# Performance work log

Hardware: AMD Instinct MI355X
Metric: run time of the kernel (lower is better)

Reference implementation:

```python
import jax, jax.numpy as jnp
import numpy as np

GRID_SIZE = 5
SPLINE_ORDER = 3
GRID_RANGE = (-1.0, 1.0)
BATCH, IN_FEATURES, OUT_FEATURES = 8192, 512, 512


def make_grid():
    h = (GRID_RANGE[1] - GRID_RANGE[0]) / GRID_SIZE
    n = GRID_SIZE + 2 * SPLINE_ORDER + 1  # 12 knots
    return jnp.linspace(GRID_RANGE[0] - SPLINE_ORDER * h,
                        GRID_RANGE[1] + SPLINE_ORDER * h,
                        n, dtype=jnp.float32)


def b_spline(x, grid, k=SPLINE_ORDER):
    # Cox-de Boor recursion. x: (B, in) -> basis: (B, in, grid_size + k)
    x = x[..., None]                     # (B, in, 1)
    g = grid[None, None, :]              # (1, 1, n_knots)
    basis = ((x >= g[..., :-1]) & (x < g[..., 1:])).astype(x.dtype)
    for p in range(1, k + 1):
        left_denom = g[..., p:-1] - g[..., :-(p + 1)]
        right_denom = g[..., p + 1:] - g[..., 1:-p]
        left_denom = jnp.where(left_denom > 0, left_denom, jnp.ones_like(left_denom))
        right_denom = jnp.where(right_denom > 0, right_denom, jnp.ones_like(right_denom))
        left = (x - g[..., :-(p + 1)]) / left_denom * basis[..., :-1]
        right = (g[..., p + 1:] - x) / right_denom * basis[..., 1:]
        basis = left + right
    return basis


def setup_inputs() -> dict:
    key = jax.random.key(0)
    k1, k2, k3 = jax.random.split(key, 3)
    # x uniform in grid_range so spline basis is active
    x = jax.random.uniform(k1, (BATCH, IN_FEATURES), jnp.float32, minval=-1.0, maxval=1.0)
    # kaiming_uniform-like init for base weight
    bound = 1.0 / np.sqrt(IN_FEATURES)
    base_weight = jax.random.uniform(k2, (OUT_FEATURES, IN_FEATURES), jnp.float32,
                                     minval=-bound, maxval=bound)
    spline_weight = jax.random.normal(k3, (OUT_FEATURES, IN_FEATURES,
                                           GRID_SIZE + SPLINE_ORDER), jnp.float32) * 0.1
    return {"x": x, "base_weight": base_weight, "spline_weight": spline_weight}


def reference(x, base_weight, spline_weight):
    grid = make_grid()
    scale_base, scale_spline = 1.0, 1.0
    base_out = x @ base_weight.T                         # (B, out)
    basis = b_spline(x, grid, SPLINE_ORDER)              # (B, in, G+k)
    spline_out = jnp.einsum('bil,oil->bo', basis, spline_weight)
    return scale_base * base_out + scale_spline * spline_out
```

## Files before the change

### kernel.cpp

```cpp
#include <hip/hip_runtime.h>
#include <stdint.h>

typedef _Float16 half8 __attribute__((ext_vector_type(8)));
typedef float floatx4 __attribute__((ext_vector_type(4)));
typedef uint32_t u32x4 __attribute__((ext_vector_type(4)));

#define BM 128
#define BN 128
#define BK 64
#define NT 512
#define KT_BASE 8
#define KT_TOTAL 72
#define IF 512
#define NF 512

__device__ __forceinline__ uint32_t swz(uint32_t b) {
  return b ^ (((b >> 7) & 7u) << 4);
}

__device__ __forceinline__ uint32_t pk(float a, float b) {
  return __builtin_bit_cast(uint32_t, __builtin_amdgcn_cvt_pkrtz(a, b));
}

__global__ __launch_bounds__(NT, 2)
void kan_fused(const float* __restrict__ xg, const float* __restrict__ bwg,
               const float* __restrict__ swg, float* __restrict__ outg)
{
  __shared__ _Float16 As[BM * BK];
  __shared__ _Float16 Bs[BN * BK];

  const int tid = threadIdx.x;
  const int lane = tid & 63;
  const int wv = tid >> 6;
  const int wm = wv >> 2;
  const int wn = wv & 3;

  const int bid = blockIdx.x;
  const int lb = (bid & 7) * 32 + (bid >> 3);
  const int bm0 = (lb & 63) * BM;
  const int bn0 = (lb >> 6) * BN;

  const int rT = tid >> 3;
  const int c8 = (tid & 7) * 8;
  const int ii = tid & 7;
  const uint32_t wA0 = swz((uint32_t)rT * 128u + (uint32_t)c8 * 2u);
  const uint32_t wA1 = swz((uint32_t)(rT + 64) * 128u + (uint32_t)c8 * 2u);

  char* AsB = (char*)As;
  char* BsB = (char*)Bs;

  uint32_t rdA[4], rdB[2];
  {
    const int rr = lane & 15;
    const uint32_t cc = (uint32_t)(lane >> 4) * 16u;
#pragma unroll
    for (int mi = 0; mi < 4; ++mi)
      rdA[mi] = swz((uint32_t)(wm * 64 + mi * 16 + rr) * 128u + cc);
#pragma unroll
    for (int ni = 0; ni < 2; ++ni)
      rdB[ni] = swz((uint32_t)(wn * 32 + ni * 16 + rr) * 128u + cc);
  }

  floatx4 acc[4][2];
#pragma unroll
  for (int mi = 0; mi < 4; ++mi)
#pragma unroll
    for (int ni = 0; ni < 2; ++ni)
      acc[mi][ni] = (floatx4){0.f, 0.f, 0.f, 0.f};

  float4 aL[4];
  float4 bL[4];
  float xv0, xv1;

  auto LOAD = [&](int kt) {
    if (kt < KT_BASE) {
      const int kb = kt * 64;
      const float* a0 = xg + (size_t)(bm0 + rT) * IF + kb + c8;
      const float* a1 = a0 + (size_t)64 * IF;
      aL[0] = ((const float4*)a0)[0]; aL[1] = ((const float4*)a0)[1];
      aL[2] = ((const float4*)a1)[0]; aL[3] = ((const float4*)a1)[1];
      const float* b0 = bwg + (size_t)(bn0 + rT) * IF + kb + c8;
      const float* b1 = b0 + (size_t)64 * IF;
      bL[0] = ((const float4*)b0)[0]; bL[1] = ((const float4*)b0)[1];
      bL[2] = ((const float4*)b1)[0]; bL[3] = ((const float4*)b1)[1];
    } else {
      const int ks = (kt - KT_BASE) * 64;
      const int i0 = ks >> 3;
      xv0 = xg[(size_t)(bm0 + rT) * IF + i0 + ii];
      xv1 = xg[(size_t)(bm0 + rT + 64) * IF + i0 + ii];
      const float* b0 = swg + (size_t)(bn0 + rT) * 4096 + ks + c8;
      const float* b1 = b0 + (size_t)64 * 4096;
      bL[0] = ((const float4*)b0)[0]; bL[1] = ((const float4*)b0)[1];
      bL[2] = ((const float4*)b1)[0]; bL[3] = ((const float4*)b1)[1];
    }
  };

  auto BASIS = [&](float xv) -> u32x4 {
    float u = (xv + 2.2f) * 2.5f;
    int j = (int)u;
    j = j < 3 ? 3 : (j > 7 ? 7 : j);
    float t = u - (float)j;
    float omt = 1.0f - t;
    float t2 = t * t, t3 = t2 * t;
    const float s6 = 0.16666666666666666f;
    float w0 = omt * omt * omt * s6;
    float w1 = (3.0f * t3 - 6.0f * t2 + 4.0f) * s6;
    float w2 = (-3.0f * t3 + 3.0f * t2 + 3.0f * t + 1.0f) * s6;
    float w3 = t3 * s6;
    uint32_t c0 = pk(w0, w1);
    uint32_t c1 = pk(w2, w3);
    const int j3 = j - 3;
    const bool odd = (j3 & 1) != 0;
    uint32_t lo  = odd ? (c0 << 16) : c0;
    uint32_t mid = odd ? ((c0 >> 16) | (c1 << 16)) : c1;
    uint32_t hi  = odd ? (c1 >> 16) : 0u;
    const int wofs = j3 >> 1;
    u32x4 r;
    r.x = (wofs == 0) ? lo : 0u;
    r.y = (wofs == 0) ? mid : ((wofs == 1) ? lo : 0u);
    r.z = (wofs == 0) ? hi : ((wofs == 1) ? mid : lo);
    r.w = (wofs == 1) ? hi : ((wofs == 2) ? mid : 0u);
    return r;
  };

  auto WRITE = [&](int kt) {
    if (kt < KT_BASE) {
      u32x4 v0; v0.x = pk(aL[0].x, aL[0].y); v0.y = pk(aL[0].z, aL[0].w);
                v0.z = pk(aL[1].x, aL[1].y); v0.w = pk(aL[1].z, aL[1].w);
      u32x4 v1; v1.x = pk(aL[2].x, aL[2].y); v1.y = pk(aL[2].z, aL[2].w);
                v1.z = pk(aL[3].x, aL[3].y); v1.w = pk(aL[3].z, aL[3].w);
      *(u32x4*)(AsB + wA0) = v0;
      *(u32x4*)(AsB + wA1) = v1;
    } else {
      *(u32x4*)(AsB + wA0) = BASIS(xv0);
      *(u32x4*)(AsB + wA1) = BASIS(xv1);
    }
    u32x4 u0; u0.x = pk(bL[0].x, bL[0].y); u0.y = pk(bL[0].z, bL[0].w);
              u0.z = pk(bL[1].x, bL[1].y); u0.w = pk(bL[1].z, bL[1].w);
    u32x4 u1; u1.x = pk(bL[2].x, bL[2].y); u1.y = pk(bL[2].z, bL[2].w);
              u1.z = pk(bL[3].x, bL[3].y); u1.w = pk(bL[3].z, bL[3].w);
    *(u32x4*)(BsB + wA0) = u0;
    *(u32x4*)(BsB + wA1) = u1;
  };

  auto COMPUTE = [&]() {
#pragma unroll
    for (int kk = 0; kk < 2; ++kk) {
      const uint32_t ko = (uint32_t)(kk * 64);
      half8 a[4], b[2];
#pragma unroll
      for (int mi = 0; mi < 4; ++mi) {
        const uint32_t off = rdA[mi] ^ ko;
        a[mi] = *(const half8*)(AsB + off);
      }
#pragma unroll
      for (int ni = 0; ni < 2; ++ni) {
        const uint32_t off = rdB[ni] ^ ko;
        b[ni] = *(const half8*)(BsB + off);
      }
#pragma unroll
      for (int mi = 0; mi < 4; ++mi)
#pragma unroll
        for (int ni = 0; ni < 2; ++ni)
          acc[mi][ni] = __builtin_amdgcn_mfma_f32_16x16x32_f16(a[mi], b[ni], acc[mi][ni], 0, 0, 0);
    }
  };

  LOAD(0);
  WRITE(0);
  __syncthreads();
#pragma unroll 1
  for (int kt = 0; kt < KT_TOTAL; ++kt) {
    const bool more = (kt + 1) < KT_TOTAL;
    if (more) LOAD(kt + 1);
    COMPUTE();
    __syncthreads();
    if (more) WRITE(kt + 1);
    __syncthreads();
  }

  const int er = (lane >> 4) * 4;
  const int ec = lane & 15;
#pragma unroll
  for (int mi = 0; mi < 4; ++mi) {
#pragma unroll
    for (int ni = 0; ni < 2; ++ni) {
      const size_t base = (size_t)(bm0 + wm * 64 + mi * 16 + er) * NF
                        + (size_t)(bn0 + wn * 32 + ni * 16 + ec);
#pragma unroll
      for (int e = 0; e < 4; ++e)
        outg[base + (size_t)e * NF] = acc[mi][ni][e];
    }
  }
}

extern "C" void kernel_launch(void* const* d_in, const int* in_sizes, int n_in,
                              void* d_out, int out_size, void* d_ws, size_t ws_size,
                              hipStream_t stream) {
  const float* x  = (const float*)d_in[0];
  const float* bw = (const float*)d_in[1];
  const float* sw = (const float*)d_in[2];
  float* out = (float*)d_out;
  hipLaunchKernelGGL(kan_fused, dim3(256), dim3(NT), 0, stream, x, bw, sw, out);
}
```

Before: 87.44 us.

## Pre-pack weights to fp16 MFMA layout and drop LDS staging with split-K atomics

Adds a prep kernel that converts base and spline weights into fp16 fragments laid out in MFMA operand order in the workspace. The main kernel then loads B fragments straight from global memory, and each wave builds its own A fragments (x converted to fp16, or B-spline basis computed in registers), so shared memory and __syncthreads disappear. The K dimension is split in two across blocks, with results combined through float atomic adds into an output that a separate kernel zeroes first. The B-spline weight formula is also simplified to use floor and FMAs. This adds two extra launches, extra weight-conversion traffic, and atomic contention on the output, and each wave rereads B from global memory or cache with no LDS sharing.

```diff
diff --git a/kernel.cpp b/kernel.cpp
--- a/kernel.cpp
+++ b/kernel.cpp
@@ -5,193 +5,165 @@
 typedef float floatx4 __attribute__((ext_vector_type(4)));
 typedef uint32_t u32x4 __attribute__((ext_vector_type(4)));
 
-#define BM 128
-#define BN 128
-#define BK 64
-#define NT 512
-#define KT_BASE 8
-#define KT_TOTAL 72
 #define IF 512
 #define NF 512
-
-__device__ __forceinline__ uint32_t swz(uint32_t b) {
-  return b ^ (((b >> 7) & 7u) << 4);
-}
+#define KT_TOTAL 72
 
 __device__ __forceinline__ uint32_t pk(float a, float b) {
   return __builtin_bit_cast(uint32_t, __builtin_amdgcn_cvt_pkrtz(a, b));
 }
 
-__global__ __launch_bounds__(NT, 2)
-void kan_fused(const float* __restrict__ xg, const float* __restrict__ bwg,
-               const float* __restrict__ swg, float* __restrict__ outg)
+__device__ __forceinline__ u32x4 BASIS8(float xv) {
+  float u = (xv + 2.2f) * 2.5f;
+  float fj = __builtin_floorf(u);
+  fj = fminf(fmaxf(fj, 3.0f), 7.0f);
+  float t = u - fj;
+  float omt = 1.0f - t;
+  float t2 = t * t, t3 = t2 * t;
+  float w0 = omt * omt * omt * 0.16666666666666666f;
+  float w1 = __builtin_fmaf(0.5f, t3, 0.66666666666666666f - t2);
+  float w2 = __builtin_fmaf(0.5f, (t2 - t3) + t, 0.16666666666666666f);
+  float w3 = t3 * 0.16666666666666666f;
+  uint32_t c0 = pk(w0, w1);
+  uint32_t c1 = pk(w2, w3);
+  int j3 = (int)fj - 3;
+  int sh = j3 << 4;
+  uint64_t w = (uint64_t)c0 | ((uint64_t)c1 << 32);
+  uint64_t lo = (sh < 64) ? (w << sh) : 0ull;
+  uint64_t hi = (sh == 0) ? 0ull : ((sh < 64) ? (w >> (64 - sh)) : w);
+  u32x4 r;
+  r.x = (uint32_t)lo; r.y = (uint32_t)(lo >> 32);
+  r.z = (uint32_t)hi; r.w = (uint32_t)(hi >> 32);
+  return r;
+}
+
+__global__ __launch_bounds__(256)
+void kan_zero(float4* __restrict__ p, int n4) {
+  const int stride = gridDim.x * 256;
+  for (int i = blockIdx.x * 256 + threadIdx.x; i < n4; i += stride)
+    p[i] = (float4){0.f, 0.f, 0.f, 0.f};
+}
+
+__global__ __launch_bounds__(256)
+void kan_prep(const float* __restrict__ bwg, const float* __restrict__ swg,
+              u32x4* __restrict__ wsB)
 {
-  __shared__ _Float16 As[BM * BK];
-  __shared__ _Float16 Bs[BN * BK];
+  const int gid = blockIdx.x * 256 + threadIdx.x;
+  const int q  = gid & 511;
+  const int Tn = gid >> 9;
+  const int kt = Tn >> 3, ns = Tn & 7;
+  const int p  = q >> 6;
+  const int hi = (q >> 4) & 3, rr = q & 15;
+  const int kk = p & 1, ni = p >> 1;
+  const int n  = ns * 64 + ni * 16 + rr;
+  const int ks = kk * 32 + hi * 8;
+  const float* src = (kt < 8) ? bwg + (size_t)n * IF + kt * 64 + ks
+                              : swg + (size_t)n * 4096 + (kt - 8) * 64 + ks;
+  float4 f0 = ((const float4*)src)[0];
+  float4 f1 = ((const float4*)src)[1];
+  u32x4 v; v.x = pk(f0.x, f0.y); v.y = pk(f0.z, f0.w);
+           v.z = pk(f1.x, f1.y); v.w = pk(f1.z, f1.w);
+  wsB[gid] = v;
+}
 
-  const int tid = threadIdx.x;
-  const int lane = tid & 63;
-  const int wv = tid >> 6;
-  const int wm = wv >> 2;
-  const int wn = wv & 3;
+__global__ __launch_bounds__(256, 4)
+void kan_fused(const float* __restrict__ xg, const uint32_t* __restrict__ wsB,
+               float* __restrict__ outg)
+{
+  const int tid = threadIdx.x, lane = tid & 63, widx = tid >> 6;
+  const int bid = blockIdx.x;
+  const int u = (bid & 7) * 128 + (bid >> 3);
+  const int ns  = u >> 7;
+  const int kz  = (u >> 6) & 1;
+  const int msb = u & 63;
+  const int ms  = msb * 4 + widx;
+  const int rr = lane & 15, hi = lane >> 4;
 
-  const int bid = blockIdx.x;
-  const int lb = (bid & 7) * 32 + (bid >> 3);
-  const int bm0 = (lb & 63) * BM;
-  const int bn0 = (lb >> 6) * BN;
+  const float* xr0 = xg + (size_t)(ms * 32 + rr) * IF;
+  const float* xr1 = xr0 + (size_t)16 * IF;
+  const char*  bbase = (const char*)wsB + (size_t)ns * 8192 + (size_t)lane * 16;
 
-  const int rT = tid >> 3;
-  const int c8 = (tid & 7) * 8;
-  const int ii = tid & 7;
-  const uint32_t wA0 = swz((uint32_t)rT * 128u + (uint32_t)c8 * 2u);
-  const uint32_t wA1 = swz((uint32_t)(rT + 64) * 128u + (uint32_t)c8 * 2u);
+  floatx4 acc[2][4];
+#pragma unroll
+  for (int mi = 0; mi < 2; ++mi)
+#pragma unroll
+    for (int ni = 0; ni < 4; ++ni)
+      acc[mi][ni] = (floatx4){0.f, 0.f, 0.f, 0.f};
 
-  char* AsB = (char*)As;
-  char* BsB = (char*)Bs;
-
-  uint32_t rdA[4], rdB[2];
-  {
-    const int rr = lane & 15;
-    const uint32_t cc = (uint32_t)(lane >> 4) * 16u;
+  if (kz == 0) {
+#pragma unroll 1
+    for (int kt = 0; kt < 8; ++kt) {
+      const char* bp = bbase + (size_t)kt * 65536;
+      u32x4 b[8];
 #pragma unroll
-    for (int mi = 0; mi < 4; ++mi)
-      rdA[mi] = swz((uint32_t)(wm * 64 + mi * 16 + rr) * 128u + cc);
+      for (int j = 0; j < 8; ++j) b[j] = *(const u32x4*)(bp + j * 1024);
 #pragma unroll
-    for (int ni = 0; ni < 2; ++ni)
-      rdB[ni] = swz((uint32_t)(wn * 32 + ni * 16 + rr) * 128u + cc);
+      for (int mi = 0; mi < 2; ++mi) {
+        const float* xr = mi ? xr1 : xr0;
+#pragma unroll
+        for (int kk = 0; kk < 2; ++kk) {
+          const float* s = xr + kt * 64 + kk * 32 + hi * 8;
+          float4 f0 = ((const float4*)s)[0];
+          float4 f1 = ((const float4*)s)[1];
+          u32x4 av; av.x = pk(f0.x, f0.y); av.y = pk(f0.z, f0.w);
+                    av.z = pk(f1.x, f1.y); av.w = pk(f1.z, f1.w);
+          half8 a = __builtin_bit_cast(half8, av);
+#pragma unroll
+          for (int ni = 0; ni < 4; ++ni)
+            acc[mi][ni] = __builtin_amdgcn_mfma_f32_16x16x32_f16(
+                a, __builtin_bit_cast(half8, b[ni * 2 + kk]), acc[mi][ni], 0, 0, 0);
+        }
+      }
+    }
   }
 
-  floatx4 acc[4][2];
+  const int ktS0 = kz ? 36 : 8, ktS1 = kz ? 72 : 36;
+  float xc[4], xn[4];
+  {
+    const int i0 = (ktS0 - 8) * 8;
 #pragma unroll
-  for (int mi = 0; mi < 4; ++mi)
+    for (int mi = 0; mi < 2; ++mi)
 #pragma unroll
-    for (int ni = 0; ni < 2; ++ni)
-      acc[mi][ni] = (floatx4){0.f, 0.f, 0.f, 0.f};
-
-  float4 aL[4];
-  float4 bL[4];
-  float xv0, xv1;
-
-  auto LOAD = [&](int kt) {
-    if (kt < KT_BASE) {
-      const int kb = kt * 64;
-      const float* a0 = xg + (size_t)(bm0 + rT) * IF + kb + c8;
-      const float* a1 = a0 + (size_t)64 * IF;
-      aL[0] = ((const float4*)a0)[0]; aL[1] = ((const float4*)a0)[1];
-      aL[2] = ((const float4*)a1)[0]; aL[3] = ((const float4*)a1)[1];
-      const float* b0 = bwg + (size_t)(bn0 + rT) * IF + kb + c8;
-      const float* b1 = b0 + (size_t)64 * IF;
-      bL[0] = ((const float4*)b0)[0]; bL[1] = ((const float4*)b0)[1];
-      bL[2] = ((const float4*)b1)[0]; bL[3] = ((const float4*)b1)[1];
-    } else {
-      const int ks = (kt - KT_BASE) * 64;
-      const int i0 = ks >> 3;
-      xv0 = xg[(size_t)(bm0 + rT) * IF + i0 + ii];
-      xv1 = xg[(size_t)(bm0 + rT + 64) * IF + i0 + ii];
-      const float* b0 = swg + (size_t)(bn0 + rT) * 4096 + ks + c8;
-      const float* b1 = b0 + (size_t)64 * 4096;
-      bL[0] = ((const float4*)b0)[0]; bL[1] = ((const float4*)b0)[1];
-      bL[2] = ((const float4*)b1)[0]; bL[3] = ((const float4*)b1)[1];
-    }
-  };
-
-  auto BASIS = [&](float xv) -> u32x4 {
-    float u = (xv + 2.2f) * 2.5f;
-    int j = (int)u;
-    j = j < 3 ? 3 : (j > 7 ? 7 : j);
-    float t = u - (float)j;
-    float omt = 1.0f - t;
-    float t2 = t * t, t3 = t2 * t;
-    const float s6 = 0.16666666666666666f;
-    float w0 = omt * omt * omt * s6;
-    float w1 = (3.0f * t3 - 6.0f * t2 + 4.0f) * s6;
-    float w2 = (-3.0f * t3 + 3.0f * t2 + 3.0f * t + 1.0f) * s6;
-    float w3 = t3 * s6;
-    uint32_t c0 = pk(w0, w1);
-    uint32_t c1 = pk(w2, w3);
-    const int j3 = j - 3;
-    const bool odd = (j3 & 1) != 0;
-    uint32_t lo  = odd ? (c0 << 16) : c0;
-    uint32_t mid = odd ? ((c0 >> 16) | (c1 << 16)) : c1;
-    uint32_t hi  = odd ? (c1 >> 16) : 0u;
-    const int wofs = j3 >> 1;
-    u32x4 r;
-    r.x = (wofs == 0) ? lo : 0u;
-    r.y = (wofs == 0) ? mid : ((wofs == 1) ? lo : 0u);
-    r.z = (wofs == 0) ? hi : ((wofs == 1) ? mid : lo);
-    r.w = (wofs == 1) ? hi : ((wofs == 2) ? mid : 0u);
-    return r;
-  };
-
-  auto WRITE = [&](int kt) {
-    if (kt < KT_BASE) {
-      u32x4 v0; v0.x = pk(aL[0].x, aL[0].y); v0.y = pk(aL[0].z, aL[0].w);
-                v0.z = pk(aL[1].x, aL[1].y); v0.w = pk(aL[1].z, aL[1].w);
-      u32x4 v1; v1.x = pk(aL[2].x, aL[2].y); v1.y = pk(aL[2].z, aL[2].w);
-                v1.z = pk(aL[3].x, aL[3].y); v1.w = pk(aL[3].z, aL[3].w);
-      *(u32x4*)(AsB + wA0) = v0;
-      *(u32x4*)(AsB + wA1) = v1;
-    } else {
-      *(u32x4*)(AsB + wA0) = BASIS(xv0);
-      *(u32x4*)(AsB + wA1) = BASIS(xv1);
-    }
-    u32x4 u0; u0.x = pk(bL[0].x, bL[0].y); u0.y = pk(bL[0].z, bL[0].w);
-              u0.z = pk(bL[1].x, bL[1].y); u0.w = pk(bL[1].z, bL[1].w);
-    u32x4 u1; u1.x = pk(bL[2].x, bL[2].y); u1.y = pk(bL[2].z, bL[2].w);
-              u1.z = pk(bL[3].x, bL[3].y); u1.w = pk(bL[3].z, bL[3].w);
-    *(u32x4*)(BsB + wA0) = u0;
-    *(u32x4*)(BsB + wA1) = u1;
-  };
-
-  auto COMPUTE = [&]() {
+      for (int kk = 0; kk < 2; ++kk)
+        xc[mi * 2 + kk] = (mi ? xr1 : xr0)[i0 + kk * 4 + hi];
+  }
+#pragma unroll 1
+  for (int kt = ktS0; kt < ktS1; ++kt) {
+    const char* bp = bbase + (size_t)kt * 65536;
+    u32x4 b[8];
 #pragma unroll
-    for (int kk = 0; kk < 2; ++kk) {
-      const uint32_t ko = (uint32_t)(kk * 64);
-      half8 a[4], b[2];
+    for (int j = 0; j < 8; ++j) b[j] = *(const u32x4*)(bp + j * 1024);
+    const int ktn = (kt + 1 < ktS1) ? (kt + 1) : kt;
+    const int i0n = (ktn - 8) * 8;
 #pragma unroll
-      for (int mi = 0; mi < 4; ++mi) {
-        const uint32_t off = rdA[mi] ^ ko;
-        a[mi] = *(const half8*)(AsB + off);
+    for (int mi = 0; mi < 2; ++mi)
+#pragma unroll
+      for (int kk = 0; kk < 2; ++kk)
+        xn[mi * 2 + kk] = (mi ? xr1 : xr0)[i0n + kk * 4 + hi];
+#pragma unroll
+    for (int mi = 0; mi < 2; ++mi)
+#pragma unroll
+      for (int kk = 0; kk < 2; ++kk) {
+        half8 a = __builtin_bit_cast(half8, BASIS8(xc[mi * 2 + kk]));
+#pragma unroll
+        for (int ni = 0; ni < 4; ++ni)
+          acc[mi][ni] = __builtin_amdgcn_mfma_f32_16x16x32_f16(
+              a, __builtin_bit_cast(half8, b[ni * 2 + kk]), acc[mi][ni], 0, 0, 0);
       }
 #pragma unroll
-      for (int ni = 0; ni < 2; ++ni) {
-        const uint32_t off = rdB[ni] ^ ko;
-        b[ni] = *(const half8*)(BsB + off);
-      }
-#pragma unroll
-      for (int mi = 0; mi < 4; ++mi)
-#pragma unroll
-        for (int ni = 0; ni < 2; ++ni)
-          acc[mi][ni] = __builtin_amdgcn_mfma_f32_16x16x32_f16(a[mi], b[ni], acc[mi][ni], 0, 0, 0);
-    }
-  };
-
-  LOAD(0);
-  WRITE(0);
-  __syncthreads();
-#pragma unroll 1
-  for (int kt = 0; kt < KT_TOTAL; ++kt) {
-    const bool more = (kt + 1) < KT_TOTAL;
-    if (more) LOAD(kt + 1);
-    COMPUTE();
-    __syncthreads();
-    if (more) WRITE(kt + 1);
-    __syncthreads();
+    for (int q2 = 0; q2 < 4; ++q2) xc[q2] = xn[q2];
   }
 
-  const int er = (lane >> 4) * 4;
-  const int ec = lane & 15;
 #pragma unroll
-  for (int mi = 0; mi < 4; ++mi) {
+  for (int mi = 0; mi < 2; ++mi)
 #pragma unroll
-    for (int ni = 0; ni < 2; ++ni) {
-      const size_t base = (size_t)(bm0 + wm * 64 + mi * 16 + er) * NF
-                        + (size_t)(bn0 + wn * 32 + ni * 16 + ec);
+    for (int ni = 0; ni < 4; ++ni) {
+      const size_t base = (size_t)(ms * 32 + mi * 16 + hi * 4) * NF
+                        + (size_t)(ns * 64 + ni * 16 + rr);
 #pragma unroll
       for (int e = 0; e < 4; ++e)
-        outg[base + (size_t)e * NF] = acc[mi][ni][e];
+        unsafeAtomicAdd(outg + base + (size_t)e * NF, acc[mi][ni][e]);
     }
-  }
 }
 
 extern "C" void kernel_launch(void* const* d_in, const int* in_sizes, int n_in,
@@ -201,5 +173,8 @@
   const float* bw = (const float*)d_in[1];
   const float* sw = (const float*)d_in[2];
   float* out = (float*)d_out;
-  hipLaunchKernelGGL(kan_fused, dim3(256), dim3(NT), 0, stream, x, bw, sw, out);
+  u32x4* wsB = (u32x4*)d_ws;
+  hipLaunchKernelGGL(kan_zero, dim3(2048), dim3(256), 0, stream, (float4*)out, out_size / 4);
+  hipLaunchKernelGGL(kan_prep, dim3(1152), dim3(256), 0, stream, bw, sw, wsB);
+  hipLaunchKernelGGL(kan_fused, dim3(1024), dim3(256), 0, stream, x, (const uint32_t*)wsB, out);
 }
```

Result: slower. 130.8 us (+49.5%).
